# Kernel optimization log

Measured on AMD Instinct MI355X. Metric: run time of the kernel, lower is better.

Reference implementation:

```python
import jax, jax.numpy as jnp
import numpy as np

B, T, C = 2, 2048, 2048
H = 16
D = C // H  # head_dim = 128


def setup_inputs() -> dict:
    key = jax.random.key(0)
    ks = jax.random.split(key, 7)
    scale = C ** -0.5
    x = jax.random.normal(ks[0], (B, T, C), dtype=jnp.float32)
    padding_mask = jax.random.randint(ks[1], (B, T), 0, 2, dtype=jnp.int32)
    Wq = jax.random.normal(ks[2], (C, C), dtype=jnp.float32) * scale
    Wk = jax.random.normal(ks[3], (C, C), dtype=jnp.float32) * scale
    Wv = jax.random.normal(ks[4], (C, C), dtype=jnp.float32) * scale
    Wp = jax.random.normal(ks[5], (C, C), dtype=jnp.float32) * scale
    bp = jax.random.normal(ks[6], (C,), dtype=jnp.float32) * 0.01
    return {"x": x, "padding_mask": padding_mask, "Wq": Wq, "Wk": Wk,
            "Wv": Wv, "Wp": Wp, "bp": bp}


def reference(x, padding_mask, Wq, Wk, Wv, Wp, bp):
    b, t, c = x.shape
    # projections (nn.Linear: x @ W.T), split heads -> [B,H,T,D]
    q = (x @ Wq.T).reshape(b, t, H, D).transpose(0, 2, 1, 3)
    k = (x @ Wk.T).reshape(b, t, H, D).transpose(0, 2, 1, 3)
    v = (x @ Wv.T).reshape(b, t, H, D).transpose(0, 2, 1, 3)
    scores = jnp.einsum('bhtd,bhsd->bhts', q, k) * (D ** -0.5)  # [B,H,T,T]
    # padding mask broadcasts along query rows: pm[b,i] masks row i (as in torch source)
    scores = jnp.where(padding_mask[:, None, :, None] == 0, jnp.float32(-1e9), scores)
    # causal mask
    causal = jnp.tril(jnp.ones((t, t), dtype=bool))
    scores = jnp.where(causal, scores, -jnp.inf)
    attn = jax.nn.softmax(scores, axis=-1)
    ctx = jnp.einsum('bhts,bhsd->bhtd', attn, v)
    ctx = ctx.transpose(0, 2, 1, 3).reshape(b, t, c)
    return ctx @ Wp.T + bp
```

## Files before the change

### kernel.cpp

```cpp
#include <hip/hip_runtime.h>
#include <stdint.h>

typedef __attribute__((ext_vector_type(8))) short vshort8;
typedef __attribute__((ext_vector_type(4))) short vshort4;
typedef __attribute__((ext_vector_type(4))) float vfloat4;

__device__ __forceinline__ short f2bf(float f) {
  union { float f; uint32_t u; } v; v.f = f;
  uint32_t r = (v.u + 0x7FFFu + ((v.u >> 16) & 1u)) >> 16;
  return (short)r;
}
__device__ __forceinline__ void gl_lds16(const void* g, void* l) {
  __builtin_amdgcn_global_load_lds(
      (const __attribute__((address_space(1))) void*)g,
      (__attribute__((address_space(3))) void*)l, 16, 0, 0);
}

__global__ void cvt_kernel(const float* __restrict__ src, short* __restrict__ dst,
                           int n) {
  int i = (blockIdx.x * blockDim.x + threadIdx.x) * 8;
  if (i >= n) return;
  vfloat4 a = *(const vfloat4*)(src + i);
  vfloat4 b = *(const vfloat4*)(src + i + 4);
  vshort8 o;
#pragma unroll
  for (int j = 0; j < 4; ++j) { o[j] = f2bf(a[j]); o[j + 4] = f2bf(b[j]); }
  *(vshort8*)(dst + i) = o;
}

__global__ void cvt4_kernel(const float* __restrict__ s0, const float* __restrict__ s1,
                            const float* __restrict__ s2, const float* __restrict__ s3,
                            short* __restrict__ d0, short* __restrict__ d1,
                            int n0, int n1) {
  const int y = blockIdx.y;
  const float* s = (y == 0) ? s0 : ((y == 1) ? s1 : ((y == 2) ? s2 : s3));
  const int n = (y == 0) ? n0 : n1;
  int i = (blockIdx.x * blockDim.x + threadIdx.x) * 8;
  if (i >= n) return;
  vfloat4 a = *(const vfloat4*)(s + i);
  vfloat4 b = *(const vfloat4*)(s + i + 4);
  vshort8 o;
#pragma unroll
  for (int j = 0; j < 4; ++j) { o[j] = f2bf(a[j]); o[j + 4] = f2bf(b[j]); }
  short* d = (y == 0) ? d0 : (d1 + (size_t)(y - 1) * n1);
  *(vshort8*)(d + i) = o;
}

#define GEMM_MAIN_LOOP()                                                        \
  const int tid  = threadIdx.x;                                                 \
  const int lane = tid & 63;                                                    \
  const int w    = tid >> 6;                                                    \
  const int wr   = w >> 2;                                                      \
  const int wc   = w & 3;                                                       \
  const int lrow = lane & 15;                                                   \
  const int quad = lane >> 4;                                                   \
  const int swz  = lrow & 7;                                                    \
  const int m0   = blockIdx.y * 128;                                            \
  const int n0   = blockIdx.x * 256;                                            \
  const int rr   = tid >> 3;                                                    \
  const int cg8  = ((tid & 7) ^ ((tid >> 3) & 7)) * 8;                          \
  const short* Ag = Aptr + (size_t)(m0 + rr) * K + cg8;                         \
  const short* Bg = Bptr + (size_t)(n0 + rr) * K + cg8;                         \
  auto stageA = [&](int bb, int kt, int i) {                                    \
    gl_lds16(Ag + (size_t)i * 64 * K + (size_t)kt * 64,                         \
             (void*)&lds[bb][i * 4096 + tid * 8]);                              \
  };                                                                            \
  auto stageB = [&](int bb, int kt, int i) {                                    \
    gl_lds16(Bg + (size_t)i * 64 * K + (size_t)kt * 64,                         \
             (void*)&lds[bb][8192 + i * 4096 + tid * 8]);                       \
  };                                                                            \
  const int aoff = (wr * 64 + lrow) * 64;                                       \
  const int boff = (wc * 64 + lrow) * 64;                                       \
  const int g8a0 = (quad ^ swz) * 8;                                            \
  const int g8a1 = ((4 + quad) ^ swz) * 8;                                      \
  vfloat4 acc[4][4] = {};                                                       \
  const int NT = K >> 6;                                                        \
  stageA(0, 0, 0); stageA(0, 0, 1);                                             \
  stageB(0, 0, 0); stageB(0, 0, 1); stageB(0, 0, 2); stageB(0, 0, 3);           \
  stageA(1, 1, 0); stageA(1, 1, 1);                                             \
  stageB(1, 1, 0); stageB(1, 1, 1); stageB(1, 1, 2); stageB(1, 1, 3);           \
  int cbuf = 0;                                                                 \
  for (int t = 0; t < NT; ++t) {                                                \
    const short* As = lds[cbuf];                                                \
    const short* Bs = lds[cbuf] + 8192;                                         \
    const int sb = (cbuf == 0) ? 2 : cbuf - 1;            \
    if (t + 1 < NT) {                                                           \
      asm volatile("s_waitcnt vmcnt(6)" ::: "memory");                          \
    } else {                                                                    \
      asm volatile("s_waitcnt vmcnt(0)" ::: "memory");                          \
    }                                                                           \
    __builtin_amdgcn_s_barrier();                                               \
    __builtin_amdgcn_sched_barrier(0);                                          \
    if (t + 2 < NT) {                                                           \
      stageA(sb, t + 2, 0); stageA(sb, t + 2, 1);                               \
      stageB(sb, t + 2, 0); stageB(sb, t + 2, 1);                               \
      stageB(sb, t + 2, 2); stageB(sb, t + 2, 3);                               \
    }                                                                           \
    vshort8 a[4][2], b[4][2];                                                   \
    _Pragma("unroll") for (int i = 0; i < 4; ++i) {                             \
      a[i][0] = *(const vshort8*)(As + aoff + i * 1024 + g8a0);                 \
      a[i][1] = *(const vshort8*)(As + aoff + i * 1024 + g8a1);                 \
      b[i][0] = *(const vshort8*)(Bs + boff + i * 1024 + g8a0);                 \
      b[i][1] = *(const vshort8*)(Bs + boff + i * 1024 + g8a1);                 \
    }                                                                           \
    __builtin_amdgcn_s_setprio(1);                                              \
    _Pragma("unroll") for (int mi = 0; mi < 4; ++mi)                            \
      _Pragma("unroll") for (int ni = 0; ni < 4; ++ni)                          \
        _Pragma("unroll") for (int ks = 0; ks < 2; ++ks)                        \
          acc[mi][ni] = __builtin_amdgcn_mfma_f32_16x16x32_bf16(                \
              a[mi][ks], b[ni][ks], acc[mi][ni], 0, 0, 0);                      \
    __builtin_amdgcn_s_setprio(0);                                              \
    __builtin_amdgcn_sched_barrier(0);                                          \
    cbuf = (cbuf == 2) ? 0 : cbuf + 1;                                          \
  }

__global__ __launch_bounds__(512, 2) void gemm_qkv(
    const short* __restrict__ Aptr, const short* __restrict__ Bptr,
    short* __restrict__ Qw, short* __restrict__ Kw, short* __restrict__ Vtw,
    int M, int K, float scale) {
  __shared__ __attribute__((aligned(16))) short lds[3][24576];
  GEMM_MAIN_LOOP()

  const int region = n0 >> 11;
#pragma unroll
  for (int mi = 0; mi < 4; ++mi) {
    int mbase = m0 + wr * 64 + mi * 16 + quad * 4;
#pragma unroll
    for (int ni = 0; ni < 4; ++ni) {
      int ng = n0 + wc * 64 + ni * 16 + lrow;
      int nn = ng & 2047;
      if (region == 2) {
        vshort4 sv;
#pragma unroll
        for (int r = 0; r < 4; ++r) sv[r] = f2bf(acc[mi][ni][r]);
        *(vshort4*)(Vtw + (size_t)nn * 4096 + mbase) = sv;
      } else if (region == 0) {
#pragma unroll
        for (int r = 0; r < 4; ++r)
          Qw[(size_t)(mbase + r) * 2048 + nn] = f2bf(acc[mi][ni][r] * scale);
      } else {
#pragma unroll
        for (int r = 0; r < 4; ++r)
          Kw[(size_t)(mbase + r) * 2048 + nn] = f2bf(acc[mi][ni][r]);
      }
    }
  }
}

__global__ __launch_bounds__(512, 2) void gemm_proj(
    const short* __restrict__ Aptr, const short* __restrict__ Bptr,
    float* __restrict__ C, const float* __restrict__ bias,
    int M, int K, int ldC) {
  __shared__ __attribute__((aligned(16))) short lds[3][24576];
  GEMM_MAIN_LOOP()

#pragma unroll
  for (int mi = 0; mi < 4; ++mi) {
    int mbase = m0 + wr * 64 + mi * 16 + quad * 4;
#pragma unroll
    for (int ni = 0; ni < 4; ++ni) {
      int n = n0 + wc * 64 + ni * 16 + lrow;
      float badd = bias[n];
#pragma unroll
      for (int r = 0; r < 4; ++r)
        C[(size_t)(mbase + r) * ldC + n] = acc[mi][ni][r] + badd;
    }
  }
}

__global__ __launch_bounds__(512, 1) void attn_kernel(
    const short* __restrict__ Q, const short* __restrict__ Kg,
    const short* __restrict__ Vt, const int* __restrict__ pm,
    short* __restrict__ ctx) {
  const int T = 2048, Cd = 2048, D = 128, MT = 4096;
  __shared__ __attribute__((aligned(16))) short Kb[3][8192];
  __shared__ __attribute__((aligned(16))) short Vb[3][8192];
  __shared__ __attribute__((aligned(16))) short Ps[8][2048];

  const int tid  = threadIdx.x;
  const int lane = tid & 63;
  const int w    = tid >> 6;
  const int lrow = lane & 15;
  const int quad = lane >> 4;
  const int qt = blockIdx.x, h = blockIdx.y, b = blockIdx.z;
  const int q0 = qt * 256 + w * 32;
  const int jmax = 4 * qt + 3;
  const int jw   = 4 * qt + (w >> 1);

  vshort8 ones;
#pragma unroll
  for (int i = 0; i < 8; ++i) ones[i] = (short)0x3F80;

  auto stage = [&](int bb, int j) {
#pragma unroll
    for (int i = 0; i < 2; ++i) {
      int s = i * 512 + tid;
      int kr = s >> 4, kg = s & 15;
      gl_lds16(Kg + (size_t)(b * T + j * 64 + kr) * Cd + h * D + (kg ^ (kr & 15)) * 8,
               (void*)&Kb[bb][s * 8]);
    }
#pragma unroll
    for (int i = 0; i < 2; ++i) {
      int s = i * 512 + tid;
      int vr = s >> 3, vg = s & 7;
      gl_lds16(Vt + (size_t)(h * D + vr) * MT + b * T + j * 64 + (vg ^ (vr & 7)) * 8,
               (void*)&Vb[bb][s * 8]);
    }
  };

  vshort8 qf[2][4];
#pragma unroll
  for (int mi = 0; mi < 2; ++mi)
#pragma unroll
    for (int ks = 0; ks < 4; ++ks)
      qf[mi][ks] = *(const vshort8*)(Q + (size_t)(b * T + q0 + mi * 16 + lrow) * Cd +
                                     h * D + ks * 32 + quad * 8);
  bool keep[2][4];
#pragma unroll
  for (int mi = 0; mi < 2; ++mi)
#pragma unroll
    for (int r = 0; r < 4; ++r)
      keep[mi][r] = pm[b * T + q0 + mi * 16 + quad * 4 + r] != 0;

  vfloat4 oacc[2][8] = {};
  vfloat4 osum[2] = {};

  stage(0, 0);
  stage(1, 1);

#pragma unroll 1
  for (int j = 0; j <= jmax; ++j) {
    if (j < jmax) {
      asm volatile("s_waitcnt vmcnt(4)" ::: "memory");
    } else {
      asm volatile("s_waitcnt vmcnt(0)" ::: "memory");
    }
    __builtin_amdgcn_s_barrier();
    __builtin_amdgcn_sched_barrier(0);
    if (j + 2 <= jmax) stage((j + 2) % 3, j + 2);

    if (j <= jw) {
      const short* Ks_ = Kb[j % 3];
      const short* Vs_ = Vb[j % 3];

      vfloat4 sacc[2][4] = {};
#pragma unroll
      for (int nt = 0; nt < 4; ++nt) {
        vshort8 kf[4];
#pragma unroll
        for (int ks = 0; ks < 4; ++ks)
          kf[ks] = *(const vshort8*)(Ks_ + (nt * 16 + lrow) * 128 +
                                     ((ks * 4 + quad) ^ lrow) * 8);
#pragma unroll
        for (int mi = 0; mi < 2; ++mi)
#pragma unroll
          for (int ks = 0; ks < 4; ++ks)
            sacc[mi][nt] = __builtin_amdgcn_mfma_f32_16x16x32_bf16(
                qf[mi][ks], kf[ks], sacc[mi][nt], 0, 0, 0);
      }

#pragma unroll
      for (int mi = 0; mi < 2; ++mi)
#pragma unroll
        for (int nt = 0; nt < 4; ++nt) {
          int s_idx = j * 64 + nt * 16 + lrow;
#pragma unroll
          for (int r = 0; r < 4; ++r) {
            int row_w = mi * 16 + quad * 4 + r;
            int qr = q0 + row_w;
            float sv = keep[mi][r] ? sacc[mi][nt][r] : 0.0f;
            float pe = __expf(sv - 12.0f);
            pe = (s_idx <= qr) ? pe : 0.0f;
            int grp = (nt * 2 + (lrow >> 3)) ^ (row_w & 7);
            Ps[w][row_w * 64 + grp * 8 + (lrow & 7)] = f2bf(pe);
          }
        }

      vshort8 pf[2][2];
#pragma unroll
      for (int mi = 0; mi < 2; ++mi)
#pragma unroll
        for (int kp = 0; kp < 2; ++kp)
          pf[mi][kp] = *(const vshort8*)(&Ps[w][(mi * 16 + lrow) * 64 +
                                               (((kp * 4 + quad) ^ (lrow & 7)) * 8)]);

#pragma unroll
      for (int mi = 0; mi < 2; ++mi)
#pragma unroll
        for (int kp = 0; kp < 2; ++kp)
          osum[mi] = __builtin_amdgcn_mfma_f32_16x16x32_bf16(pf[mi][kp], ones, osum[mi], 0, 0, 0);

#pragma unroll
      for (int dt = 0; dt < 8; ++dt) {
        vshort8 vf0 = *(const vshort8*)(Vs_ + (dt * 16 + lrow) * 64 +
                                        (quad ^ (lrow & 7)) * 8);
        vshort8 vf1 = *(const vshort8*)(Vs_ + (dt * 16 + lrow) * 64 +
                                        ((4 + quad) ^ (lrow & 7)) * 8);
#pragma unroll
        for (int mi = 0; mi < 2; ++mi) {
          oacc[mi][dt] = __builtin_amdgcn_mfma_f32_16x16x32_bf16(pf[mi][0], vf0, oacc[mi][dt], 0, 0, 0);
          oacc[mi][dt] = __builtin_amdgcn_mfma_f32_16x16x32_bf16(pf[mi][1], vf1, oacc[mi][dt], 0, 0, 0);
        }
      }
    }
  }

#pragma unroll
  for (int mi = 0; mi < 2; ++mi) {
    float il[4];
#pragma unroll
    for (int r = 0; r < 4; ++r)
      il[r] = __builtin_amdgcn_rcpf(fmaxf(osum[mi][r], 1e-30f));
#pragma unroll
    for (int dt = 0; dt < 8; ++dt) {
      int d = dt * 16 + lrow;
#pragma unroll
      for (int r = 0; r < 4; ++r) {
        float o = oacc[mi][dt][r] * il[r];
        ctx[(size_t)(b * T + q0 + mi * 16 + quad * 4 + r) * Cd + h * D + d] = f2bf(o);
      }
    }
  }
}

extern "C" void kernel_launch(void* const* d_in, const int* in_sizes, int n_in,
                              void* d_out, int out_size, void* d_ws, size_t ws_size,
                              hipStream_t stream) {
  (void)in_sizes; (void)n_in; (void)out_size; (void)ws_size;
  const float* x  = (const float*)d_in[0];
  const int*   pm = (const int*)d_in[1];
  const float* Wq = (const float*)d_in[2];
  const float* Wk = (const float*)d_in[3];
  const float* Wv = (const float*)d_in[4];
  const float* Wp = (const float*)d_in[5];
  const float* bp = (const float*)d_in[6];
  float* out = (float*)d_out;

  const int Bb = 2, T = 2048, Cd = 2048, M = Bb * T;
  const size_t SZ = (size_t)M * Cd;
  const size_t WZ = (size_t)Cd * Cd;
  short* xb   = (short*)d_ws;
  short* Qw   = xb + SZ;
  short* Kw   = Qw + SZ;
  short* Vtw  = Kw + SZ;
  short* Cx   = Vtw + SZ;
  short* wcat = Cx + SZ;

  const int CB = 256;
  dim3 gw(((int)WZ / 8 + CB - 1) / CB);
  const float scale = 0.08838834764831845f;

  cvt4_kernel<<<dim3(((int)SZ / 8 + CB - 1) / CB, 4), CB, 0, stream>>>(
      x, Wq, Wk, Wv, xb, wcat, (int)SZ, (int)WZ);

  gemm_qkv<<<dim3(6144 / 256, M / 128), 512, 0, stream>>>(
      xb, wcat, Qw, Kw, Vtw, M, Cd, scale);

  cvt_kernel<<<gw, CB, 0, stream>>>(Wp, xb, (int)WZ);

  attn_kernel<<<dim3(8, 16, Bb), 512, 0, stream>>>(Qw, Kw, Vtw, pm, Cx);

  gemm_proj<<<dim3(Cd / 256, M / 128), 512, 0, stream>>>(Cx, xb, out, bp, M, Cd, Cd);
}
```

Measured before the change: 377.2 us.

## Rebalance causal attention by pairing query tiles and loading V directly

New measurement: 407.4 us. 1.08x slower.

```diff
diff --git a/kernel.cpp b/kernel.cpp
--- a/kernel.cpp
+++ b/kernel.cpp
@@ -168,156 +168,158 @@
   }
 }
 
-__global__ __launch_bounds__(512, 1) void attn_kernel(
+__global__ __launch_bounds__(256, 1) void attn_kernel(
     const short* __restrict__ Q, const short* __restrict__ Kg,
     const short* __restrict__ Vt, const int* __restrict__ pm,
     short* __restrict__ ctx) {
   const int T = 2048, Cd = 2048, D = 128, MT = 4096;
   __shared__ __attribute__((aligned(16))) short Kb[3][8192];
-  __shared__ __attribute__((aligned(16))) short Vb[3][8192];
-  __shared__ __attribute__((aligned(16))) short Ps[8][2048];
+  __shared__ __attribute__((aligned(16))) short Ps[4][32][72];
 
   const int tid  = threadIdx.x;
   const int lane = tid & 63;
   const int w    = tid >> 6;
   const int lrow = lane & 15;
   const int quad = lane >> 4;
-  const int qt = blockIdx.x, h = blockIdx.y, b = blockIdx.z;
-  const int q0 = qt * 256 + w * 32;
-  const int jmax = 4 * qt + 3;
-  const int jw   = 4 * qt + (w >> 1);
+  const int hb = blockIdx.x;
+  const int pb = blockIdx.y;
+  const int b = hb >> 4, h = hb & 15;
 
   vshort8 ones;
 #pragma unroll
   for (int i = 0; i < 8; ++i) ones[i] = (short)0x3F80;
 
-  auto stage = [&](int bb, int j) {
-#pragma unroll
-    for (int i = 0; i < 2; ++i) {
-      int s = i * 512 + tid;
+  auto stageK = [&](int bb, int j) {
+#pragma unroll
+    for (int i = 0; i < 4; ++i) {
+      int s = i * 256 + tid;
       int kr = s >> 4, kg = s & 15;
       gl_lds16(Kg + (size_t)(b * T + j * 64 + kr) * Cd + h * D + (kg ^ (kr & 15)) * 8,
                (void*)&Kb[bb][s * 8]);
     }
-#pragma unroll
-    for (int i = 0; i < 2; ++i) {
-      int s = i * 512 + tid;
-      int vr = s >> 3, vg = s & 7;
-      gl_lds16(Vt + (size_t)(h * D + vr) * MT + b * T + j * 64 + (vg ^ (vr & 7)) * 8,
-               (void*)&Vb[bb][s * 8]);
-    }
   };
 
-  vshort8 qf[2][4];
-#pragma unroll
-  for (int mi = 0; mi < 2; ++mi)
-#pragma unroll
-    for (int ks = 0; ks < 4; ++ks)
-      qf[mi][ks] = *(const vshort8*)(Q + (size_t)(b * T + q0 + mi * 16 + lrow) * Cd +
-                                     h * D + ks * 32 + quad * 8);
-  bool keep[2][4];
-#pragma unroll
-  for (int mi = 0; mi < 2; ++mi)
-#pragma unroll
-    for (int r = 0; r < 4; ++r)
-      keep[mi][r] = pm[b * T + q0 + mi * 16 + quad * 4 + r] != 0;
-
-  vfloat4 oacc[2][8] = {};
-  vfloat4 osum[2] = {};
-
-  stage(0, 0);
-  stage(1, 1);
-
 #pragma unroll 1
-  for (int j = 0; j <= jmax; ++j) {
-    if (j < jmax) {
-      asm volatile("s_waitcnt vmcnt(4)" ::: "memory");
-    } else {
-      asm volatile("s_waitcnt vmcnt(0)" ::: "memory");
-    }
+  for (int tt = 0; tt < 2; ++tt) {
+    const int qt = tt ? (15 - pb) : pb;
+    const int q0 = qt * 128 + w * 32;
+    const int jmax = 2 * qt + 1;
+    const int jw = (q0 + 31) >> 6;
+
+    vshort8 qf[2][4];
+#pragma unroll
+    for (int mi = 0; mi < 2; ++mi)
+#pragma unroll
+      for (int ks = 0; ks < 4; ++ks)
+        qf[mi][ks] = *(const vshort8*)(Q + (size_t)(b * T + q0 + mi * 16 + lrow) * Cd +
+                                       h * D + ks * 32 + quad * 8);
+    bool keep[2];
+#pragma unroll
+    for (int mi = 0; mi < 2; ++mi)
+      keep[mi] = pm[b * T + q0 + mi * 16 + lrow] != 0;
+
+    vfloat4 oacc[2][8] = {};
+    vfloat4 osum[2] = {};
+
     __builtin_amdgcn_s_barrier();
-    __builtin_amdgcn_sched_barrier(0);
-    if (j + 2 <= jmax) stage((j + 2) % 3, j + 2);
-
-    if (j <= jw) {
-      const short* Ks_ = Kb[j % 3];
-      const short* Vs_ = Vb[j % 3];
-
-      vfloat4 sacc[2][4] = {};
-#pragma unroll
-      for (int nt = 0; nt < 4; ++nt) {
-        vshort8 kf[4];
-#pragma unroll
-        for (int ks = 0; ks < 4; ++ks)
-          kf[ks] = *(const vshort8*)(Ks_ + (nt * 16 + lrow) * 128 +
-                                     ((ks * 4 + quad) ^ lrow) * 8);
-#pragma unroll
-        for (int mi = 0; mi < 2; ++mi)
+    stageK(0, 0);
+    stageK(1, 1);
+
+#pragma unroll 1
+    for (int j = 0; j <= jmax; ++j) {
+      if (j + 2 <= jmax) {
+        stageK((j + 2) % 3, j + 2);
+        asm volatile("s_waitcnt vmcnt(8)" ::: "memory");
+      } else if (j + 1 <= jmax) {
+        asm volatile("s_waitcnt vmcnt(4)" ::: "memory");
+      } else {
+        asm volatile("s_waitcnt vmcnt(0)" ::: "memory");
+      }
+      __builtin_amdgcn_s_barrier();
+      __builtin_amdgcn_sched_barrier(0);
+
+      if (j <= jw) {
+        vshort8 vf[8][2];
+#pragma unroll
+        for (int dt = 0; dt < 8; ++dt)
+#pragma unroll
+          for (int kp = 0; kp < 2; ++kp)
+            vf[dt][kp] = *(const vshort8*)(Vt + (size_t)(h * D + dt * 16 + lrow) * MT +
+                                           b * T + j * 64 + kp * 32 + quad * 8);
+
+        const short* Ks_ = Kb[j % 3];
+        vfloat4 sacc[2][4] = {};
+#pragma unroll
+        for (int nt = 0; nt < 4; ++nt) {
+          vshort8 kf[4];
 #pragma unroll
           for (int ks = 0; ks < 4; ++ks)
-            sacc[mi][nt] = __builtin_amdgcn_mfma_f32_16x16x32_bf16(
-                qf[mi][ks], kf[ks], sacc[mi][nt], 0, 0, 0);
-      }
-
-#pragma unroll
-      for (int mi = 0; mi < 2; ++mi)
-#pragma unroll
-        for (int nt = 0; nt < 4; ++nt) {
-          int s_idx = j * 64 + nt * 16 + lrow;
-#pragma unroll
-          for (int r = 0; r < 4; ++r) {
-            int row_w = mi * 16 + quad * 4 + r;
-            int qr = q0 + row_w;
-            float sv = keep[mi][r] ? sacc[mi][nt][r] : 0.0f;
-            float pe = __expf(sv - 12.0f);
-            pe = (s_idx <= qr) ? pe : 0.0f;
-            int grp = (nt * 2 + (lrow >> 3)) ^ (row_w & 7);
-            Ps[w][row_w * 64 + grp * 8 + (lrow & 7)] = f2bf(pe);
+            kf[ks] = *(const vshort8*)(Ks_ + (nt * 16 + lrow) * 128 +
+                                       ((ks * 4 + quad) ^ lrow) * 8);
+#pragma unroll
+          for (int mi = 0; mi < 2; ++mi)
+#pragma unroll
+            for (int ks = 0; ks < 4; ++ks)
+              sacc[mi][nt] = __builtin_amdgcn_mfma_f32_16x16x32_bf16(
+                  kf[ks], qf[mi][ks], sacc[mi][nt], 0, 0, 0);
+        }
+
+#pragma unroll
+        for (int mi = 0; mi < 2; ++mi) {
+          const int qm = q0 + mi * 16 + lrow;
+          const bool kp_ = keep[mi];
+#pragma unroll
+          for (int nt = 0; nt < 4; ++nt) {
+            vshort4 sv4;
+#pragma unroll
+            for (int r = 0; r < 4; ++r) {
+              int kv = j * 64 + nt * 16 + quad * 4 + r;
+              float sv = kp_ ? sacc[mi][nt][r] : 0.0f;
+              float pe = __expf(sv - 12.0f);
+              pe = (kv <= qm) ? pe : 0.0f;
+              sv4[r] = f2bf(pe);
+            }
+            *(vshort4*)(&Ps[w][mi * 16 + lrow][nt * 16 + quad * 4]) = sv4;
           }
         }
 
-      vshort8 pf[2][2];
-#pragma unroll
-      for (int mi = 0; mi < 2; ++mi)
-#pragma unroll
-        for (int kp = 0; kp < 2; ++kp)
-          pf[mi][kp] = *(const vshort8*)(&Ps[w][(mi * 16 + lrow) * 64 +
-                                               (((kp * 4 + quad) ^ (lrow & 7)) * 8)]);
-
-#pragma unroll
-      for (int mi = 0; mi < 2; ++mi)
-#pragma unroll
-        for (int kp = 0; kp < 2; ++kp)
-          osum[mi] = __builtin_amdgcn_mfma_f32_16x16x32_bf16(pf[mi][kp], ones, osum[mi], 0, 0, 0);
-
+        vshort8 pf[2][2];
+#pragma unroll
+        for (int mi = 0; mi < 2; ++mi)
+#pragma unroll
+          for (int kp = 0; kp < 2; ++kp)
+            pf[mi][kp] = *(const vshort8*)(&Ps[w][mi * 16 + lrow][kp * 32 + quad * 8]);
+
+#pragma unroll
+        for (int mi = 0; mi < 2; ++mi)
+#pragma unroll
+          for (int kp = 0; kp < 2; ++kp)
+            osum[mi] = __builtin_amdgcn_mfma_f32_16x16x32_bf16(pf[mi][kp], ones, osum[mi], 0, 0, 0);
+
+#pragma unroll
+        for (int dt = 0; dt < 8; ++dt)
+#pragma unroll
+          for (int mi = 0; mi < 2; ++mi) {
+            oacc[mi][dt] = __builtin_amdgcn_mfma_f32_16x16x32_bf16(pf[mi][0], vf[dt][0], oacc[mi][dt], 0, 0, 0);
+            oacc[mi][dt] = __builtin_amdgcn_mfma_f32_16x16x32_bf16(pf[mi][1], vf[dt][1], oacc[mi][dt], 0, 0, 0);
+          }
+      }
+    }
+
+#pragma unroll
+    for (int mi = 0; mi < 2; ++mi) {
+      float il[4];
+#pragma unroll
+      for (int r = 0; r < 4; ++r)
+        il[r] = __builtin_amdgcn_rcpf(fmaxf(osum[mi][r], 1e-30f));
 #pragma unroll
       for (int dt = 0; dt < 8; ++dt) {
-        vshort8 vf0 = *(const vshort8*)(Vs_ + (dt * 16 + lrow) * 64 +
-                                        (quad ^ (lrow & 7)) * 8);
-        vshort8 vf1 = *(const vshort8*)(Vs_ + (dt * 16 + lrow) * 64 +
-                                        ((4 + quad) ^ (lrow & 7)) * 8);
-#pragma unroll
-        for (int mi = 0; mi < 2; ++mi) {
-          oacc[mi][dt] = __builtin_amdgcn_mfma_f32_16x16x32_bf16(pf[mi][0], vf0, oacc[mi][dt], 0, 0, 0);
-          oacc[mi][dt] = __builtin_amdgcn_mfma_f32_16x16x32_bf16(pf[mi][1], vf1, oacc[mi][dt], 0, 0, 0);
+        int d = dt * 16 + lrow;
+#pragma unroll
+        for (int r = 0; r < 4; ++r) {
+          float o = oacc[mi][dt][r] * il[r];
+          ctx[(size_t)(b * T + q0 + mi * 16 + quad * 4 + r) * Cd + h * D + d] = f2bf(o);
         }
-      }
-    }
-  }
-
-#pragma unroll
-  for (int mi = 0; mi < 2; ++mi) {
-    float il[4];
-#pragma unroll
-    for (int r = 0; r < 4; ++r)
-      il[r] = __builtin_amdgcn_rcpf(fmaxf(osum[mi][r], 1e-30f));
-#pragma unroll
-    for (int dt = 0; dt < 8; ++dt) {
-      int d = dt * 16 + lrow;
-#pragma unroll
-      for (int r = 0; r < 4; ++r) {
-        float o = oacc[mi][dt][r] * il[r];
-        ctx[(size_t)(b * T + q0 + mi * 16 + quad * 4 + r) * Cd + h * D + d] = f2bf(o);
       }
     }
   }
@@ -358,7 +360,7 @@
 
   cvt_kernel<<<gw, CB, 0, stream>>>(Wp, xb, (int)WZ);
 
-  attn_kernel<<<dim3(8, 16, Bb), 512, 0, stream>>>(Qw, Kw, Vtw, pm, Cx);
+  attn_kernel<<<dim3(32, 8), 256, 0, stream>>>(Qw, Kw, Vtw, pm, Cx);
 
   gemm_proj<<<dim3(Cd / 256, M / 128), 512, 0, stream>>>(Cx, xb, out, bp, M, Cd, Cd);
 }
```
